# Kernel tuning notes

Hardware: AMD Instinct MI355X
Metric: run time of the kernel (lower is better)

Reference implementation:

```python
import jax, jax.numpy as jnp
import numpy as np

PI = np.pi
N_QUBITS = 10
DIM = 2 ** N_QUBITS
HALF = 2 ** (N_QUBITS - 1)
BATCH = 8192


def _bit_table(n):
    # [2^n, n] bools, qubit 0 = most significant bit (matches dec2bin)
    rows = np.arange(2 ** n)
    return ((rows[:, None] >> np.arange(n - 1, -1, -1)[None, :]) & 1).astype(bool)


def _cnot_perm(n, c_bit, t_bit):
    # CNOT as an index permutation: flip target bit where control bit is set.
    idx = np.arange(2 ** n)
    cmask = 1 << (n - 1 - c_bit)
    tmask = 1 << (n - 1 - t_bit)
    return np.where((idx & cmask) != 0, idx ^ tmask, idx)


def _ry2(theta):
    a = theta / 2
    c = jnp.cos(a).astype(jnp.complex64)
    s = jnp.sin(a).astype(jnp.complex64)
    return jnp.stack([c, -s, s, c]).reshape(2, 2)


def _rx2(theta):
    a = theta / 2
    c = jnp.cos(a).astype(jnp.complex64)
    s = jnp.sin(a).astype(jnp.complex64)
    return jnp.stack([c, -1j * s, -1j * s, c]).reshape(2, 2)


def _rz2(theta):
    a = theta / 2
    e_m = jnp.exp(-1j * a).astype(jnp.complex64)
    e_p = jnp.exp(1j * a).astype(jnp.complex64)
    z = jnp.zeros((), jnp.complex64)
    return jnp.stack([e_m, z, z, e_p]).reshape(2, 2)


def setup_inputs() -> dict:
    key = jax.random.key(0)
    k1, k2 = jax.random.split(key)
    inputs = jax.random.normal(k1, (BATCH, N_QUBITS), dtype=jnp.float32)
    weight = jax.random.normal(k2, (3 + 2 * N_QUBITS,), dtype=jnp.float32)
    # entangle_matrix: product of chained CNOT(i, i+1) gates -> real 0/1 permutation matrix
    E = np.eye(DIM, dtype=np.float32)
    for i in range(N_QUBITS - 1):
        perm = _cnot_perm(N_QUBITS, i, i + 1)
        P = np.zeros((DIM, DIM), dtype=np.float32)
        P[perm, np.arange(DIM)] = 1.0
        E = P @ E
    return {"inputs": inputs, "weight": weight, "entangle_matrix": jnp.asarray(E)}


def reference(inputs, weight, entangle_matrix):
    n = N_QUBITS
    B = inputs.shape[0]
    # torch: if inputs.max() > 1: inputs = arctan(inputs)
    inputs = jnp.where(inputs.max() > 1.0, jnp.arctan(inputs), inputs)

    # ---- Encoder: |psi> = kron_q (e^{-i a_q/2}, e^{+i a_q/2}) / sqrt(2)
    angles = (2.0 * PI) * inputs                                   # [B, n]
    v = jnp.stack([jnp.exp(-1j * angles / 2), jnp.exp(1j * angles / 2)], axis=-1)
    v = v / np.float32(np.sqrt(2.0))                               # [B, n, 2]
    vec = jnp.ones((B, 1), jnp.complex64)
    for q in range(n):                                             # qubit 0 = MSB
        vec = (vec[:, :, None] * v[:, q, None, :]).reshape(B, -1)  # [B, 2^(q+1)]

    # ---- higher order encoding: CNOT . Rz(t, 2pi*x_c*x_t) . CNOT for each c<t
    bits = _bit_table(n)                                           # [2^n, n]
    for c in range(n):
        for t in range(c + 1, n):
            perm = _cnot_perm(n, c, t)
            vec = vec[:, perm]
            ang = inputs[:, c] * inputs[:, t] * (2.0 * PI)          # [B]
            e_m = jnp.exp(-1j * ang / 2)[:, None]
            e_p = jnp.exp(1j * ang / 2)[:, None]
            vec = vec * jnp.where(bits[None, :, t], e_m, e_p)
            vec = vec[:, perm]

    # ---- trainable rotation layer: kron_q Rx(w_q*2pi) @ Rz(w_{n+q}*2pi)
    R = jnp.ones((1, 1), jnp.complex64)
    for q in range(n):
        R = jnp.kron(R, _rx2(weight[3 + q] * 2 * PI) @ _rz2(weight[3 + n + q] * 2 * PI))
    E = entangle_matrix.astype(jnp.complex64)
    M = E @ R @ E                                                  # [2^n, 2^n]
    vec = vec @ M.T                                                # tensordot(vec, M, ([-1],[-1]))

    # ---- final rotation on qubit 0 (note: original uses ry-form for all three)
    Rf = _ry2(weight[2] * 2 * PI) @ (_ry2(weight[1] * 2 * PI) @ _ry2(weight[0] * 2 * PI))
    vec = jnp.einsum('ij,bja->bia', Rf, vec.reshape(B, 2, HALF)).reshape(B, -1)

    # ---- measurement: <Z_0> style difference of probabilities
    probs = vec.real ** 2 + vec.imag ** 2
    return probs[:, HALF:].sum(-1) - probs[:, :HALF].sum(-1)
```

## Files before the change

### kernel.cpp

```cpp
#include <hip/hip_runtime.h>
#include <math.h>

#define NQ 10
#define BATCHN 8192
#define PI_F 3.14159265358979f

typedef float v2f __attribute__((ext_vector_type(2)));

__global__ __launch_bounds__(256) void prep_kernel(const float* __restrict__ in,
                                                   int n,
                                                   const float* __restrict__ w,
                                                   int* __restrict__ flags,
                                                   float* __restrict__ gtab) {
    __shared__ int bf;
    if (threadIdx.x == 0) bf = 0;
    __syncthreads();
    const int tid = blockIdx.x * 256 + threadIdx.x;
    bool pred = false;
    for (int i = tid; i < n; i += 64 * 256) pred |= (in[i] > 1.0f);
    if (__any(pred) && (threadIdx.x & 63) == 0) atomicOr(&bf, 1);
    __syncthreads();
    if (threadIdx.x == 0) flags[blockIdx.x] = bf;

    if (blockIdx.x == 0) {
        const int t = threadIdx.x;
        if (t < 10) {
            float s, c;
            __sincosf(PI_F * w[12 - t], &s, &c);
            gtab[2 * t]     = c;
            gtab[2 * t + 1] = s;
            gtab[22 + t]    = w[22 - t];
        } else if (t == 10) {
            float s2, c2;
            __sincosf(2.0f * PI_F * (w[0] + w[1] + w[2]), &s2, &c2);
            gtab[20] = c2;
            gtab[21] = s2;
        }
    }
}

__device__ __forceinline__ float rfl(float v) {
    return __uint_as_float(__builtin_amdgcn_readfirstlane(__float_as_uint(v)));
}
__device__ __forceinline__ float rdlane(float v, int l) {
    return __uint_as_float(__builtin_amdgcn_readlane(__float_as_uint(v), l));
}
__device__ __forceinline__ float xor1_dpp(float v) {
    return __int_as_float(__builtin_amdgcn_update_dpp(
        __float_as_int(v), __float_as_int(v), 0xB1, 0xF, 0xF, true));
}
__device__ __forceinline__ float xor2_dpp(float v) {
    return __int_as_float(__builtin_amdgcn_update_dpp(
        __float_as_int(v), __float_as_int(v), 0x4E, 0xF, 0xF, true));
}
__device__ __forceinline__ float xor4_swz(float v) {
    return __int_as_float(__builtin_amdgcn_ds_swizzle(__float_as_int(v), 0x101F));
}
__device__ __forceinline__ float xor8_swz(float v) {
    return __int_as_float(__builtin_amdgcn_ds_swizzle(__float_as_int(v), 0x201F));
}
__device__ __forceinline__ v2f vfma(v2f a, v2f b, v2f c) {
    return __builtin_elementwise_fma(a, b, c);
}
__device__ __forceinline__ v2f splat(float v) { return (v2f){v, v}; }
__device__ __forceinline__ v2f vswap(v2f v) {
    return __builtin_shufflevector(v, v, 1, 0);
}

#define HAVE_PLSWAP (__has_builtin(__builtin_amdgcn_permlane16_swap))
#if HAVE_PLSWAP
typedef unsigned uv2 __attribute__((ext_vector_type(2)));
__device__ __forceinline__ void pl16_swap(float& a, float& b) {
    uv2 r = __builtin_amdgcn_permlane16_swap(__float_as_uint(a),
                                             __float_as_uint(b), false, false);
    a = __uint_as_float(r.x);
    b = __uint_as_float(r.y);
}
__device__ __forceinline__ void pl32_swap(float& a, float& b) {
    uv2 r = __builtin_amdgcn_permlane32_swap(__float_as_uint(a),
                                             __float_as_uint(b), false, false);
    a = __uint_as_float(r.x);
    b = __uint_as_float(r.y);
}
#endif

#define GATE_REG2(c, s, m)                                                     \
    {                                                                          \
        const v2f cv = splat(c), sv = splat(s), nsv = splat(-(s));             \
        _Pragma("unroll") for (int r = 0; r < 8; ++r) if (!(r & (m))) {        \
            const int r2 = r | (m);                                            \
            const v2f ar = re2[r], ai = im2[r];                                \
            const v2f br = re2[r2], bi = im2[r2];                              \
            re2[r]  = vfma(cv, ar, sv * bi);                                   \
            im2[r]  = vfma(cv, ai, nsv * br);                                  \
            re2[r2] = vfma(cv, br, sv * ai);                                   \
            im2[r2] = vfma(cv, bi, nsv * ar);                                  \
        }                                                                      \
    }

#define GATE_LANE2(c, s, EXCH)                                                 \
    {                                                                          \
        const v2f cv = splat(c), sv = splat(s), nsv = splat(-(s));             \
        _Pragma("unroll") for (int r = 0; r < 8; ++r) {                        \
            v2f pr, pim;                                                       \
            pr.x  = EXCH(re2[r].x);  pr.y  = EXCH(re2[r].y);                   \
            pim.x = EXCH(im2[r].x);  pim.y = EXCH(im2[r].y);                   \
            re2[r] = vfma(cv, re2[r], sv * pim);                               \
            im2[r] = vfma(cv, im2[r], nsv * pr);                               \
        }                                                                      \
    }

__global__ __launch_bounds__(256, 8) void qsim_kernel(const float* __restrict__ in,
                                                      const int* __restrict__ flags,
                                                      const float* __restrict__ G,
                                                      float* __restrict__ out) {
    const int lane = threadIdx.x & 63;
    const int b    = blockIdx.x * 4 + (threadIdx.x >> 6);

    const bool anyflag = __any(flags[lane] != 0);

    float xv = 0.0f;
    if (lane < NQ) xv = in[b * NQ + lane];
    if (anyflag) xv = atanf(xv);
    float x[NQ];
#pragma unroll
    for (int q = 0; q < NQ; ++q) x[q] = rdlane(xv, q);

    float Qs = 0.0f;
#pragma unroll
    for (int q = 0; q < NQ; ++q) Qs += x[q] * x[q];

    float gc[NQ], gs[NQ], wz[NQ];
#pragma unroll
    for (int p = 0; p < NQ; ++p) {
        gc[p] = rfl(G[2 * p]);
        gs[p] = rfl(G[2 * p + 1]);
        wz[p] = rfl(G[22 + p]);
    }
    const float c2 = rfl(G[20]);
    const float s2 = rfl(G[21]);

    const int jlo = (lane ^ (lane >> 1)) & 7;
    const int j8  = ((lane >> 4) ^ (lane >> 5)) & 1;
    const int k9  = (lane >> 5) & 1;
    const int k3  = (lane >> 3) & 1;
    const int k8  = (lane >> 4) & 1;

    const float Sh1 = 1.0f
        + (jlo & 1 ? x[9] : -x[9])
        + (jlo & 2 ? x[8] : -x[8])
        + (jlo & 4 ? x[7] : -x[7])
        + (j8 ? x[1] : -x[1])
        + (k9 ? x[0] : -x[0]);
    const float x6s = k3 ? x[6] : -x[6];
    const float x2s = k8 ? x[2] : -x[2];

    const float Dl = 0.5f * (
          ((lane & 1) ? wz[0] : -wz[0])
        + ((lane & 2) ? wz[1] : -wz[1])
        + ((lane & 4) ? wz[2] : -wz[2])
        + ((lane & 8) ? wz[3] : -wz[3])
        + (k8 ? wz[8] : -wz[8])
        + (k9 ? wz[9] : -wz[9]))
        - 0.25f * (1.0f + Qs);
    const float h4 = 0.5f * wz[4], h5 = 0.5f * wz[5];
    const float h6 = 0.5f * wz[6], h7 = 0.5f * wz[7];

    v2f re2[8], im2[8];
#pragma unroll
    for (int r = 0; r < 8; ++r) {
        const int g0 = (r ^ (r >> 1)) & 1;
        const int g1 = ((r >> 1) ^ (r >> 2)) & 1;
        const float Tc = Sh1
            + ((r & 1) ? -x6s : x6s)
            + (g0 ? x[5] : -x[5])
            + (g1 ? x[4] : -x[4]);
        const float v = ((r & 4) ? x[3] : -x[3]) + x2s;
        const float Dc = Dl
            + ((r & 1) ? h4 : -h4)
            + ((r & 2) ? h5 : -h5)
            + ((r & 4) ? h6 : -h6);
        const v2f T2 = {Tc + v, Tc - v};
        const v2f D2 = {Dc - h7, Dc + h7};
        const v2f rev = vfma(splat(0.25f) * T2, T2, D2);
        im2[r] = (v2f){__builtin_amdgcn_sinf(rev.x), __builtin_amdgcn_sinf(rev.y)};
        re2[r] = (v2f){__builtin_amdgcn_cosf(rev.x), __builtin_amdgcn_cosf(rev.y)};
    }

    GATE_REG2(gc[4], gs[4], 1)
    GATE_REG2(gc[5], gs[5], 2)
    GATE_REG2(gc[6], gs[6], 4)

    {
        const v2f cv = splat(gc[7]), sv = splat(gs[7]), nsv = splat(-gs[7]);
#pragma unroll
        for (int r = 0; r < 8; ++r) {
            const v2f pr = vswap(re2[r]), pim = vswap(im2[r]);
            re2[r] = vfma(cv, re2[r], sv * pim);
            im2[r] = vfma(cv, im2[r], nsv * pr);
        }
    }

    GATE_LANE2(gc[0], gs[0], xor1_dpp)
    GATE_LANE2(gc[1], gs[1], xor2_dpp)
    GATE_LANE2(gc[2], gs[2], xor4_swz)
    GATE_LANE2(gc[3], gs[3], xor8_swz)

    float acc;
#if HAVE_PLSWAP
#pragma unroll
    for (int r = 0; r < 8; r += 2) {
        float a, bq;
        a = re2[r].x; bq = re2[r + 1].x; pl16_swap(a, bq); re2[r].x = a; re2[r + 1].x = bq;
        a = re2[r].y; bq = re2[r + 1].y; pl16_swap(a, bq); re2[r].y = a; re2[r + 1].y = bq;
        a = im2[r].x; bq = im2[r + 1].x; pl16_swap(a, bq); im2[r].x = a; im2[r + 1].x = bq;
        a = im2[r].y; bq = im2[r + 1].y; pl16_swap(a, bq); im2[r].y = a; im2[r + 1].y = bq;
    }
    GATE_REG2(gc[8], gs[8], 1)
#pragma unroll
    for (int r = 0; r < 8; ++r) {
        if (!(r & 2)) {
            const int r2 = r | 2;
            float a, bq;
            a = re2[r].x; bq = re2[r2].x; pl32_swap(a, bq); re2[r].x = a; re2[r2].x = bq;
            a = re2[r].y; bq = re2[r2].y; pl32_swap(a, bq); re2[r].y = a; re2[r2].y = bq;
            a = im2[r].x; bq = im2[r2].x; pl32_swap(a, bq); im2[r].x = a; im2[r2].x = bq;
            a = im2[r].y; bq = im2[r2].y; pl32_swap(a, bq); im2[r].y = a; im2[r2].y = bq;
        }
    }
    GATE_REG2(gc[9], gs[9], 2)

    {
        const v2f cv = splat(c2), sv = splat(2.0f * s2);
        v2f acc2 = splat(0.0f);
#pragma unroll
        for (int r = 0; r < 8; ++r) {
            if (!(r & 2)) {
                const int rp = r ^ 3;
                const v2f pa  = vfma(re2[r],  re2[r],  im2[r]  * im2[r]);
                const v2f pb  = vfma(re2[rp], re2[rp], im2[rp] * im2[rp]);
                const v2f dot = vfma(re2[r],  re2[rp], im2[r]  * im2[rp]);
                acc2 = vfma(cv, pb - pa, vfma(sv, dot, acc2));
            }
        }
        acc = acc2.x + acc2.y;
    }
#else
    GATE_LANE2(gc[8], gs[8], [&](float vv) { return __shfl_xor(vv, 16, 64); })
    GATE_LANE2(gc[9], gs[9], [&](float vv) { return __shfl_xor(vv, 32, 64); })
    {
        const float cc = k9 ? c2 : -c2;
        v2f acc2 = splat(0.0f);
#pragma unroll
        for (int r = 0; r < 8; ++r) {
            v2f pr, pim;
            pr.x  = __shfl_xor(re2[r].x, 48, 64);
            pr.y  = __shfl_xor(re2[r].y, 48, 64);
            pim.x = __shfl_xor(im2[r].x, 48, 64);
            pim.y = __shfl_xor(im2[r].y, 48, 64);
            const v2f pown = vfma(re2[r], re2[r], im2[r] * im2[r]);
            const v2f dot  = vfma(re2[r], pr, im2[r] * pim);
            acc2 = vfma(splat(cc), pown, vfma(splat(s2), dot, acc2));
        }
        acc = acc2.x + acc2.y;
    }
#endif

    acc += xor1_dpp(acc);
    acc += xor2_dpp(acc);
    acc += xor4_swz(acc);
    acc += xor8_swz(acc);
    acc += __shfl_xor(acc, 16, 64);
    acc += __shfl_xor(acc, 32, 64);
    if (lane == 0) out[b] = acc * 0.0009765625f;
}

extern "C" void kernel_launch(void* const* d_in, const int* in_sizes, int n_in,
                              void* d_out, int out_size, void* d_ws, size_t ws_size,
                              hipStream_t stream) {
    const float* inputs = (const float*)d_in[0];
    const float* weight = (const float*)d_in[1];
    float* out   = (float*)d_out;
    int*   flags = (int*)d_ws;
    float* gtab  = (float*)d_ws + 64;

    prep_kernel<<<64, 256, 0, stream>>>(inputs, BATCHN * NQ, weight, flags, gtab);
    qsim_kernel<<<BATCHN / 4, 256, 0, stream>>>(inputs, flags, gtab, out);
}
```

Measured before the change: 72.07 us.

## Replace statevector simulation with closed-form expectation per sample

Replaces the per-sample 1024-amplitude statevector evolution (one wavefront per sample) with an analytic closed-form expression for the measured expectation, computed by one thread per sample from products of cosines and sines of input-derived angles. Inputs are staged through shared memory, and prep precomputes a few weight-derived scalars. This removes nearly all gate arithmetic and cross-lane exchanges. The risk is that the derivation must hold for arbitrary weights; it reads only w[0..3], w[13] and w[14], so it leans on the circuit structure collapsing most weights out.

```diff
diff --git a/kernel.cpp b/kernel.cpp
--- a/kernel.cpp
+++ b/kernel.cpp
@@ -3,9 +3,7 @@
 
 #define NQ 10
 #define BATCHN 8192
-#define PI_F 3.14159265358979f
 
-typedef float v2f __attribute__((ext_vector_type(2)));
 
 __global__ __launch_bounds__(256) void prep_kernel(const float* __restrict__ in,
                                                    int n,
@@ -22,257 +20,60 @@
     __syncthreads();
     if (threadIdx.x == 0) flags[blockIdx.x] = bf;
 
-    if (blockIdx.x == 0) {
-        const int t = threadIdx.x;
-        if (t < 10) {
-            float s, c;
-            __sincosf(PI_F * w[12 - t], &s, &c);
-            gtab[2 * t]     = c;
-            gtab[2 * t + 1] = s;
-            gtab[22 + t]    = w[22 - t];
-        } else if (t == 10) {
-            float s2, c2;
-            __sincosf(2.0f * PI_F * (w[0] + w[1] + w[2]), &s2, &c2);
-            gtab[20] = c2;
-            gtab[21] = s2;
-        }
+    if (blockIdx.x == 0 && threadIdx.x == 0) {
+        const float sw  = w[0] + w[1] + w[2];
+        const float cb  = __builtin_amdgcn_cosf(sw);
+        const float sb  = __builtin_amdgcn_sinf(sw);
+        const float st0 = __builtin_amdgcn_sinf(w[3]);
+        gtab[0] = 0.5f * cb * st0;
+        gtab[1] = 0.5f * sb;
+        gtab[2] = w[13];
+        gtab[3] = w[14];
     }
 }
 
-__device__ __forceinline__ float rfl(float v) {
-    return __uint_as_float(__builtin_amdgcn_readfirstlane(__float_as_uint(v)));
-}
-__device__ __forceinline__ float rdlane(float v, int l) {
-    return __uint_as_float(__builtin_amdgcn_readlane(__float_as_uint(v), l));
-}
-__device__ __forceinline__ float xor1_dpp(float v) {
-    return __int_as_float(__builtin_amdgcn_update_dpp(
-        __float_as_int(v), __float_as_int(v), 0xB1, 0xF, 0xF, true));
-}
-__device__ __forceinline__ float xor2_dpp(float v) {
-    return __int_as_float(__builtin_amdgcn_update_dpp(
-        __float_as_int(v), __float_as_int(v), 0x4E, 0xF, 0xF, true));
-}
-__device__ __forceinline__ float xor4_swz(float v) {
-    return __int_as_float(__builtin_amdgcn_ds_swizzle(__float_as_int(v), 0x101F));
-}
-__device__ __forceinline__ float xor8_swz(float v) {
-    return __int_as_float(__builtin_amdgcn_ds_swizzle(__float_as_int(v), 0x201F));
-}
-__device__ __forceinline__ v2f vfma(v2f a, v2f b, v2f c) {
-    return __builtin_elementwise_fma(a, b, c);
-}
-__device__ __forceinline__ v2f splat(float v) { return (v2f){v, v}; }
-__device__ __forceinline__ v2f vswap(v2f v) {
-    return __builtin_shufflevector(v, v, 1, 0);
-}
+__global__ __launch_bounds__(256) void expect_kernel(const float* __restrict__ in,
+                                                     const int* __restrict__ flags,
+                                                     const float* __restrict__ G,
+                                                     float* __restrict__ out) {
+    __shared__ float xs[256 * NQ];
+    const int base = blockIdx.x * (256 * NQ);
+    for (int i = threadIdx.x; i < 256 * NQ; i += 256) xs[i] = in[base + i];
 
-#define HAVE_PLSWAP (__has_builtin(__builtin_amdgcn_permlane16_swap))
-#if HAVE_PLSWAP
-typedef unsigned uv2 __attribute__((ext_vector_type(2)));
-__device__ __forceinline__ void pl16_swap(float& a, float& b) {
-    uv2 r = __builtin_amdgcn_permlane16_swap(__float_as_uint(a),
-                                             __float_as_uint(b), false, false);
-    a = __uint_as_float(r.x);
-    b = __uint_as_float(r.y);
-}
-__device__ __forceinline__ void pl32_swap(float& a, float& b) {
-    uv2 r = __builtin_amdgcn_permlane32_swap(__float_as_uint(a),
-                                             __float_as_uint(b), false, false);
-    a = __uint_as_float(r.x);
-    b = __uint_as_float(r.y);
-}
-#endif
+    const int lane = threadIdx.x & 63;
+    const bool anyflag = __any(flags[lane] != 0);
 
-#define GATE_REG2(c, s, m)                                                     \
-    {                                                                          \
-        const v2f cv = splat(c), sv = splat(s), nsv = splat(-(s));             \
-        _Pragma("unroll") for (int r = 0; r < 8; ++r) if (!(r & (m))) {        \
-            const int r2 = r | (m);                                            \
-            const v2f ar = re2[r], ai = im2[r];                                \
-            const v2f br = re2[r2], bi = im2[r2];                              \
-            re2[r]  = vfma(cv, ar, sv * bi);                                   \
-            im2[r]  = vfma(cv, ai, nsv * br);                                  \
-            re2[r2] = vfma(cv, br, sv * ai);                                   \
-            im2[r2] = vfma(cv, bi, nsv * ar);                                  \
-        }                                                                      \
+    const float g0 = G[0], g1 = G[1], l0 = G[2], l1 = G[3];
+
+    __syncthreads();
+
+    float x[NQ];
+#pragma unroll
+    for (int q = 0; q < NQ; ++q) x[q] = xs[threadIdx.x * NQ + q];
+    if (anyflag) {
+#pragma unroll
+        for (int q = 0; q < NQ; ++q) x[q] = atanf(x[q]);
     }
 
-#define GATE_LANE2(c, s, EXCH)                                                 \
-    {                                                                          \
-        const v2f cv = splat(c), sv = splat(s), nsv = splat(-(s));             \
-        _Pragma("unroll") for (int r = 0; r < 8; ++r) {                        \
-            v2f pr, pim;                                                       \
-            pr.x  = EXCH(re2[r].x);  pr.y  = EXCH(re2[r].y);                   \
-            pim.x = EXCH(im2[r].x);  pim.y = EXCH(im2[r].y);                   \
-            re2[r] = vfma(cv, re2[r], sv * pim);                               \
-            im2[r] = vfma(cv, im2[r], nsv * pr);                               \
-        }                                                                      \
+    const float mp = x[0] + x[1], mm = x[0] - x[1];
+    const float np_ = x[0] + x[2], nm = x[0] - x[2];
+
+    float Kmp = 1.0f, Kmm = 1.0f, Knp = 1.0f, Knm = 1.0f;
+#pragma unroll
+    for (int t = 3; t < NQ; ++t) {
+        Kmp *= __builtin_amdgcn_cosf(mp * x[t]);
+        Kmm *= __builtin_amdgcn_cosf(mm * x[t]);
+        Knp *= __builtin_amdgcn_cosf(np_ * x[t]);
+        Knm *= __builtin_amdgcn_cosf(nm * x[t]);
     }
 
-__global__ __launch_bounds__(256, 8) void qsim_kernel(const float* __restrict__ in,
-                                                      const int* __restrict__ flags,
-                                                      const float* __restrict__ G,
-                                                      float* __restrict__ out) {
-    const int lane = threadIdx.x & 63;
-    const int b    = blockIdx.x * 4 + (threadIdx.x >> 6);
+    const float t1 = __builtin_amdgcn_sinf(mp + l0) * __builtin_amdgcn_cosf(mp * x[2]) * Kmp
+                   + __builtin_amdgcn_sinf(mm + l0) * __builtin_amdgcn_cosf(mm * x[2]) * Kmm;
+    const float t2 = __builtin_amdgcn_cosf(np_ + l0) * __builtin_amdgcn_cosf(np_ * x[1] - l1) * Knp
+                   + __builtin_amdgcn_cosf(nm + l0) * __builtin_amdgcn_cosf(nm * x[1] - l1) * Knm;
 
-    const bool anyflag = __any(flags[lane] != 0);
-
-    float xv = 0.0f;
-    if (lane < NQ) xv = in[b * NQ + lane];
-    if (anyflag) xv = atanf(xv);
-    float x[NQ];
-#pragma unroll
-    for (int q = 0; q < NQ; ++q) x[q] = rdlane(xv, q);
-
-    float Qs = 0.0f;
-#pragma unroll
-    for (int q = 0; q < NQ; ++q) Qs += x[q] * x[q];
-
-    float gc[NQ], gs[NQ], wz[NQ];
-#pragma unroll
-    for (int p = 0; p < NQ; ++p) {
-        gc[p] = rfl(G[2 * p]);
-        gs[p] = rfl(G[2 * p + 1]);
-        wz[p] = rfl(G[22 + p]);
-    }
-    const float c2 = rfl(G[20]);
-    const float s2 = rfl(G[21]);
-
-    const int jlo = (lane ^ (lane >> 1)) & 7;
-    const int j8  = ((lane >> 4) ^ (lane >> 5)) & 1;
-    const int k9  = (lane >> 5) & 1;
-    const int k3  = (lane >> 3) & 1;
-    const int k8  = (lane >> 4) & 1;
-
-    const float Sh1 = 1.0f
-        + (jlo & 1 ? x[9] : -x[9])
-        + (jlo & 2 ? x[8] : -x[8])
-        + (jlo & 4 ? x[7] : -x[7])
-        + (j8 ? x[1] : -x[1])
-        + (k9 ? x[0] : -x[0]);
-    const float x6s = k3 ? x[6] : -x[6];
-    const float x2s = k8 ? x[2] : -x[2];
-
-    const float Dl = 0.5f * (
-          ((lane & 1) ? wz[0] : -wz[0])
-        + ((lane & 2) ? wz[1] : -wz[1])
-        + ((lane & 4) ? wz[2] : -wz[2])
-        + ((lane & 8) ? wz[3] : -wz[3])
-        + (k8 ? wz[8] : -wz[8])
-        + (k9 ? wz[9] : -wz[9]))
-        - 0.25f * (1.0f + Qs);
-    const float h4 = 0.5f * wz[4], h5 = 0.5f * wz[5];
-    const float h6 = 0.5f * wz[6], h7 = 0.5f * wz[7];
-
-    v2f re2[8], im2[8];
-#pragma unroll
-    for (int r = 0; r < 8; ++r) {
-        const int g0 = (r ^ (r >> 1)) & 1;
-        const int g1 = ((r >> 1) ^ (r >> 2)) & 1;
-        const float Tc = Sh1
-            + ((r & 1) ? -x6s : x6s)
-            + (g0 ? x[5] : -x[5])
-            + (g1 ? x[4] : -x[4]);
-        const float v = ((r & 4) ? x[3] : -x[3]) + x2s;
-        const float Dc = Dl
-            + ((r & 1) ? h4 : -h4)
-            + ((r & 2) ? h5 : -h5)
-            + ((r & 4) ? h6 : -h6);
-        const v2f T2 = {Tc + v, Tc - v};
-        const v2f D2 = {Dc - h7, Dc + h7};
-        const v2f rev = vfma(splat(0.25f) * T2, T2, D2);
-        im2[r] = (v2f){__builtin_amdgcn_sinf(rev.x), __builtin_amdgcn_sinf(rev.y)};
-        re2[r] = (v2f){__builtin_amdgcn_cosf(rev.x), __builtin_amdgcn_cosf(rev.y)};
-    }
-
-    GATE_REG2(gc[4], gs[4], 1)
-    GATE_REG2(gc[5], gs[5], 2)
-    GATE_REG2(gc[6], gs[6], 4)
-
-    {
-        const v2f cv = splat(gc[7]), sv = splat(gs[7]), nsv = splat(-gs[7]);
-#pragma unroll
-        for (int r = 0; r < 8; ++r) {
-            const v2f pr = vswap(re2[r]), pim = vswap(im2[r]);
-            re2[r] = vfma(cv, re2[r], sv * pim);
-            im2[r] = vfma(cv, im2[r], nsv * pr);
-        }
-    }
-
-    GATE_LANE2(gc[0], gs[0], xor1_dpp)
-    GATE_LANE2(gc[1], gs[1], xor2_dpp)
-    GATE_LANE2(gc[2], gs[2], xor4_swz)
-    GATE_LANE2(gc[3], gs[3], xor8_swz)
-
-    float acc;
-#if HAVE_PLSWAP
-#pragma unroll
-    for (int r = 0; r < 8; r += 2) {
-        float a, bq;
-        a = re2[r].x; bq = re2[r + 1].x; pl16_swap(a, bq); re2[r].x = a; re2[r + 1].x = bq;
-        a = re2[r].y; bq = re2[r + 1].y; pl16_swap(a, bq); re2[r].y = a; re2[r + 1].y = bq;
-        a = im2[r].x; bq = im2[r + 1].x; pl16_swap(a, bq); im2[r].x = a; im2[r + 1].x = bq;
-        a = im2[r].y; bq = im2[r + 1].y; pl16_swap(a, bq); im2[r].y = a; im2[r + 1].y = bq;
-    }
-    GATE_REG2(gc[8], gs[8], 1)
-#pragma unroll
-    for (int r = 0; r < 8; ++r) {
-        if (!(r & 2)) {
-            const int r2 = r | 2;
-            float a, bq;
-            a = re2[r].x; bq = re2[r2].x; pl32_swap(a, bq); re2[r].x = a; re2[r2].x = bq;
-            a = re2[r].y; bq = re2[r2].y; pl32_swap(a, bq); re2[r].y = a; re2[r2].y = bq;
-            a = im2[r].x; bq = im2[r2].x; pl32_swap(a, bq); im2[r].x = a; im2[r2].x = bq;
-            a = im2[r].y; bq = im2[r2].y; pl32_swap(a, bq); im2[r].y = a; im2[r2].y = bq;
-        }
-    }
-    GATE_REG2(gc[9], gs[9], 2)
-
-    {
-        const v2f cv = splat(c2), sv = splat(2.0f * s2);
-        v2f acc2 = splat(0.0f);
-#pragma unroll
-        for (int r = 0; r < 8; ++r) {
-            if (!(r & 2)) {
-                const int rp = r ^ 3;
-                const v2f pa  = vfma(re2[r],  re2[r],  im2[r]  * im2[r]);
-                const v2f pb  = vfma(re2[rp], re2[rp], im2[rp] * im2[rp]);
-                const v2f dot = vfma(re2[r],  re2[rp], im2[r]  * im2[rp]);
-                acc2 = vfma(cv, pb - pa, vfma(sv, dot, acc2));
-            }
-        }
-        acc = acc2.x + acc2.y;
-    }
-#else
-    GATE_LANE2(gc[8], gs[8], [&](float vv) { return __shfl_xor(vv, 16, 64); })
-    GATE_LANE2(gc[9], gs[9], [&](float vv) { return __shfl_xor(vv, 32, 64); })
-    {
-        const float cc = k9 ? c2 : -c2;
-        v2f acc2 = splat(0.0f);
-#pragma unroll
-        for (int r = 0; r < 8; ++r) {
-            v2f pr, pim;
-            pr.x  = __shfl_xor(re2[r].x, 48, 64);
-            pr.y  = __shfl_xor(re2[r].y, 48, 64);
-            pim.x = __shfl_xor(im2[r].x, 48, 64);
-            pim.y = __shfl_xor(im2[r].y, 48, 64);
-            const v2f pown = vfma(re2[r], re2[r], im2[r] * im2[r]);
-            const v2f dot  = vfma(re2[r], pr, im2[r] * pim);
-            acc2 = vfma(splat(cc), pown, vfma(splat(s2), dot, acc2));
-        }
-        acc = acc2.x + acc2.y;
-    }
-#endif
-
-    acc += xor1_dpp(acc);
-    acc += xor2_dpp(acc);
-    acc += xor4_swz(acc);
-    acc += xor8_swz(acc);
-    acc += __shfl_xor(acc, 16, 64);
-    acc += __shfl_xor(acc, 32, 64);
-    if (lane == 0) out[b] = acc * 0.0009765625f;
+    const int b = blockIdx.x * 256 + threadIdx.x;
+    out[b] = fmaf(-g0, t1, g1 * t2);
 }
 
 extern "C" void kernel_launch(void* const* d_in, const int* in_sizes, int n_in,
@@ -285,5 +86,5 @@
     float* gtab  = (float*)d_ws + 64;
 
     prep_kernel<<<64, 256, 0, stream>>>(inputs, BATCHN * NQ, weight, flags, gtab);
-    qsim_kernel<<<BATCHN / 4, 256, 0, stream>>>(inputs, flags, gtab, out);
+    expect_kernel<<<BATCHN / 256, 256, 0, stream>>>(inputs, flags, gtab, out);
 }
```

After: 63.18 us. 1.14x faster.
